# Kernel tuning notes

Measured on AMD Instinct MI355X. Metric: run time of the kernel, lower is better.

## Reference

```python
import jax, jax.numpy as jnp
import numpy as np

B, N, DIM = 4, 2048, 512
H, DH = 8, 64  # heads, dim_head; inner_dim = H*DH = 512


def setup_inputs() -> dict:
    key = jax.random.key(0)
    ks = jax.random.split(key, 7)
    s = 0.02
    return {
        "x": jax.random.normal(ks[0], (B, N, DIM), dtype=jnp.float32),
        "w_qkv": jax.random.normal(ks[1], (DIM, 3 * H * DH), dtype=jnp.float32) * s,
        "b_qkv": jnp.zeros((3 * H * DH,), dtype=jnp.float32),
        "th1": jax.random.normal(ks[2], (H, H), dtype=jnp.float32) * (1.0 / H) + jnp.eye(H, dtype=jnp.float32),
        "th2": jax.random.normal(ks[3], (H, H), dtype=jnp.float32) * (1.0 / H) + jnp.eye(H, dtype=jnp.float32),
        "w_out": jax.random.normal(ks[4], (H * DH, DIM), dtype=jnp.float32) * s,
        "b_out": jnp.zeros((DIM,), dtype=jnp.float32),
    }


def reference(x, w_qkv, b_qkv, th1, th2, w_out, b_out):
    b, n, _ = x.shape
    scale = DH ** -0.5
    qkv = x @ w_qkv + b_qkv                       # [b, n, 3*H*DH]
    q, k, v = jnp.split(qkv, 3, axis=-1)
    to_heads = lambda t: t.reshape(b, n, H, DH).transpose(0, 2, 1, 3)  # b h n d
    q, k, v = to_heads(q), to_heads(k), to_heads(v)
    dots = jnp.einsum('bhnd,bhmd->bhnm', q, k) * scale   # [b, h, n, n]
    dots = jnp.einsum('gh,bhnm->bgnm', th1, dots)        # talking-heads pre-softmax (1x1 conv over heads)
    attn = jax.nn.softmax(dots, axis=-1)
    attn = jnp.einsum('gh,bhnm->bgnm', th2, attn)        # talking-heads post-softmax
    out = jnp.einsum('bhnm,bhmd->bhnd', attn, v)         # [b, h, n, d]
    out = out.transpose(0, 2, 1, 3).reshape(b, n, H * DH)
    return out @ w_out + b_out
```

## Files before the change

### kernel.cpp

```cpp
#include <hip/hip_runtime.h>

typedef _Float16 half8  __attribute__((ext_vector_type(8)));
typedef _Float16 half4  __attribute__((ext_vector_type(4)));
typedef float    f32x4  __attribute__((ext_vector_type(4)));

#define MFMA32(a,b,c) __builtin_amdgcn_mfma_f32_16x16x32_f16(a,b,c,0,0,0)
#define MFMA16(a,b,c) __builtin_amdgcn_mfma_f32_16x16x16f16(a,b,c,0,0,0)

#if __has_builtin(__builtin_amdgcn_exp2f)
#define EXP2F(x) __builtin_amdgcn_exp2f(x)
#else
#define EXP2F(x) exp2f(x)
#endif

#define GLOAD16(gp, lp) __builtin_amdgcn_global_load_lds(                      \
    (const __attribute__((address_space(1))) void*)(gp),                       \
    (__attribute__((address_space(3))) void*)(lp), 16, 0, 0)

static constexpr float SCALE_LOG2E = 0.18033688011112042f;

static constexpr size_t QH_OFF = 0;
static constexpr size_t KH_OFF = (size_t)8  << 20;
static constexpr size_t VT_OFF = (size_t)16 << 20;
static constexpr size_t LS_OFF = (size_t)24 << 20;
static constexpr size_t O_OFF  = (size_t)25 << 20;
static constexpr size_t LPART  = (size_t)4*8*2048;
static constexpr size_t OPART  = (size_t)8192*512;

static constexpr int GS = 340;

__global__ __launch_bounds__(256)
void k_cvtx(const float* __restrict__ x, _Float16* __restrict__ xf)
{
  const size_t i = ((size_t)blockIdx.x*256 + threadIdx.x)*4;
  f32x4 v = *(const f32x4*)(x + i);
  half4 h;
#pragma unroll
  for (int j = 0; j < 4; j++) h[j] = (_Float16)v[j];
  *(half4*)(xf + i) = h;
}

__global__ __launch_bounds__(256)
void k_cvtw(const float* __restrict__ w, _Float16* __restrict__ wt)
{
  __shared__ _Float16 T[32][36];
  const int kt = blockIdx.x, ct = blockIdx.y;
  const int r = threadIdx.x >> 3, c4 = (threadIdx.x & 7)*4;
  f32x4 v = *(const f32x4*)(w + (size_t)(kt*32 + r)*1536 + ct*32 + c4);
#pragma unroll
  for (int j = 0; j < 4; j++) T[r][c4 + j] = (_Float16)v[j];
  __syncthreads();
  half4 o;
#pragma unroll
  for (int j = 0; j < 4; j++) o[j] = T[c4 + j][r];
  *(half4*)(wt + (size_t)(ct*32 + r)*512 + kt*32 + c4) = o;
}

__global__ __launch_bounds__(256)
void k_qkv(const _Float16* __restrict__ xf, const _Float16* __restrict__ wt,
           const float* __restrict__ bias, _Float16* __restrict__ Qh,
           _Float16* __restrict__ Kh, _Float16* __restrict__ Vt)
{
  __shared__ __align__(16) _Float16 Xs[2048];
  __shared__ __align__(16) _Float16 Ws[2048];
  const int tid = threadIdx.x;
  const int wv = tid >> 6, lane = tid & 63, l15 = lane & 15, qd = lane >> 4;
  const int row0 = blockIdx.x * 64, col0 = blockIdx.y * 64;

  const int sslot = wv*64 + lane;
  const int sr = sslot >> 2, so = (sslot & 3) ^ ((sr >> 1) & 3);

  f32x4 acc[4] = {{0.f,0.f,0.f,0.f},{0.f,0.f,0.f,0.f},{0.f,0.f,0.f,0.f},{0.f,0.f,0.f,0.f}};

  for (int k0 = 0; k0 < 512; k0 += 32) {
    GLOAD16(xf + (size_t)(row0 + sr)*512 + k0 + so*8, &Xs[wv*512]);
    GLOAD16(wt + (size_t)(col0 + sr)*512 + k0 + so*8, &Ws[wv*512]);
    __syncthreads();
    const int ra = wv*16 + l15;
    half8 af = *(const half8*)&Xs[(ra*4 + (qd ^ ((ra >> 1) & 3)))*8];
#pragma unroll
    for (int ct = 0; ct < 4; ct++) {
      const int rb = ct*16 + l15;
      half8 bf = *(const half8*)&Ws[(rb*4 + (qd ^ ((rb >> 1) & 3)))*8];
      acc[ct] = MFMA32(af, bf, acc[ct]);
    }
    __syncthreads();
  }
#pragma unroll
  for (int ct = 0; ct < 4; ct++) {
    const int c = col0 + ct*16 + l15;
    const int sec = c >> 9, hh = (c >> 6) & 7, d = c & 63;
    const float bv = bias[c];
#pragma unroll
    for (int i = 0; i < 4; i++) {
      const int row = row0 + wv*16 + qd*4 + i;
      const int bb = row >> 11, n = row & 2047;
      float v = acc[ct][i] + bv;
      if (sec == 0)
        Qh[((size_t)((bb*8 + hh)*2048 + n))*64 + d] = (_Float16)(v * SCALE_LOG2E);
      else if (sec == 1)
        Kh[((size_t)((bb*8 + hh)*2048 + n))*64 + d] = (_Float16)v;
      else
        Vt[((size_t)((bb*8 + hh)*64 + d))*2048 + n] = (_Float16)v;
    }
  }
}

__global__ __launch_bounds__(512, 4)
void k_pass1(const _Float16* __restrict__ Qh, const _Float16* __restrict__ Kh,
             const float* __restrict__ th1, float* __restrict__ Lsum)
{
  __shared__ __align__(16) _Float16 KB[8][1024];
  __shared__ __align__(16) _Float16 Sb[2][2][2704];
  const int tid = threadIdx.x;
  const int wv = tid >> 6, lane = tid & 63, l15 = lane & 15, qd = lane >> 4;
  const int s = blockIdx.x & 7, nt = blockIdx.x >> 3;
  const int b = s >> 1, mh = s & 1;
  const int n0 = nt << 5;
  const _Float16* kbase = Kh + ((size_t)((b*8 + wv)*2048 + mh*1024))*64;

  half4 a1f;
#pragma unroll
  for (int j = 0; j < 4; j++)
    a1f[j] = ((l15 >> 3) == (qd >> 1)) ? (_Float16)th1[(l15 & 7)*8 + (qd & 1)*4 + j]
                                       : (_Float16)0.f;

  half8 qf[2][2];
#pragma unroll
  for (int t = 0; t < 2; t++) {
    const _Float16* qp = Qh + ((size_t)((b*8 + wv)*2048 + n0 + t*16 + l15))*64 + qd*8;
    qf[t][0] = *(const half8*)qp;
    qf[t][1] = *(const half8*)(qp + 32);
  }

  auto issueK = [&](int it) {
#pragma unroll
    for (int j = 0; j < 2; j++) {
      const int bk = j*64 + lane;
      const int m = bk >> 3, c = bk & 7;
      const int cp = c ^ (m & 7);
      GLOAD16(kbase + (size_t)(it*16 + m)*64 + cp*8, &KB[wv][j*512]);
    }
  };
  auto qk_to_sb = [&](int buf) {
    half8 ka0 = *(const half8*)&KB[wv][l15*64 + ((qd       ^ (l15 & 7))*8)];
    half8 ka1 = *(const half8*)&KB[wv][l15*64 + (((4 + qd) ^ (l15 & 7))*8)];
#pragma unroll
    for (int t = 0; t < 2; t++) {
      f32x4 a = {0.f,0.f,0.f,0.f};
      a = MFMA32(ka0, qf[t][0], a);
      a = MFMA32(ka1, qf[t][1], a);
#pragma unroll
      for (int i = 0; i < 4; i++)
        Sb[buf][t][(l15 >> 1)*GS + (qd*4 + i)*20 + wv + 8*(l15 & 1)] = (_Float16)a[i];
    }
  };

  float lacc[2][4];
#pragma unroll
  for (int t = 0; t < 2; t++)
#pragma unroll
    for (int i = 0; i < 4; i++) lacc[t][i] = 0.f;

  issueK(0);
  __syncthreads();
  for (int it = 0; it <= 64; it++) {
    if (it < 64) {
      qk_to_sb(it & 1);
      if (it + 1 < 64) issueK(it + 1);
    }
    if (it >= 1) {
      const int buf = (it - 1) & 1;
#pragma unroll
      for (int t = 0; t < 2; t++) {
        half4 b1 = *(const half4*)&Sb[buf][t][wv*GS + l15*20 + qd*4];
        f32x4 c1 = MFMA16(a1f, b1, ((f32x4){0.f,0.f,0.f,0.f}));
#pragma unroll
        for (int i = 0; i < 4; i++) lacc[t][i] += EXP2F(c1[i]);
      }
    }
    __syncthreads();
  }

#pragma unroll
  for (int t = 0; t < 2; t++)
#pragma unroll
    for (int i = 0; i < 4; i++) {
      float v = lacc[t][i];
      v += __shfl_xor(v, 1); v += __shfl_xor(v, 2);
      v += __shfl_xor(v, 4); v += __shfl_xor(v, 8);
      lacc[t][i] = v;
    }
  if (l15 == 0) {
#pragma unroll
    for (int t = 0; t < 2; t++)
#pragma unroll
      for (int i = 0; i < 4; i++) {
        const int n = n0 + t*16 + wv*2 + (qd >> 1);
        const int g = (qd & 1)*4 + i;
        Lsum[(size_t)mh*LPART + (size_t)(b*8 + g)*2048 + n] = lacc[t][i];
      }
  }
}

__global__ __launch_bounds__(512, 4)
void k_pass2(const _Float16* __restrict__ Qh, const _Float16* __restrict__ Kh,
             const _Float16* __restrict__ Vt, const float* __restrict__ Lsum,
             const float* __restrict__ th1, const float* __restrict__ th2,
             _Float16* __restrict__ Obuf)
{
  __shared__ __align__(16) _Float16 KB[8][1024];
  __shared__ __align__(16) _Float16 VB[8][1024];
  __shared__ __align__(16) _Float16 Sb[2][2][2704];
  __shared__ __align__(16) _Float16 Wb[2][2][2704];
  const int tid = threadIdx.x;
  const int wv = tid >> 6, lane = tid & 63, l15 = lane & 15, qd = lane >> 4;
  const int s = blockIdx.x & 7, nt = blockIdx.x >> 3;
  const int b = s >> 1, mh = s & 1;
  const int n0 = nt << 5;
  const _Float16* kbase = Kh + ((size_t)((b*8 + wv)*2048 + mh*1024))*64;
  const _Float16* vbase = Vt + (size_t)(b*8 + wv)*64*2048 + mh*1024;

  half4 a1f, b2f;
#pragma unroll
  for (int j = 0; j < 4; j++) {
    const bool diag = ((l15 >> 3) == (qd >> 1));
    a1f[j] = diag ? (_Float16)th1[(l15 & 7)*8 + (qd & 1)*4 + j] : (_Float16)0.f;
    b2f[j] = diag ? (_Float16)th2[(l15 & 7)*8 + (qd & 1)*4 + j] : (_Float16)0.f;
  }

  f32x4 cs[2];
#pragma unroll
  for (int t = 0; t < 2; t++)
#pragma unroll
    for (int i = 0; i < 4; i++) {
      const int n = n0 + t*16 + wv*2 + (qd >> 1);
      const int g = (qd & 1)*4 + i;
      const size_t off = (size_t)(b*8 + g)*2048 + n;
      cs[t][i] = -__log2f(Lsum[off] + Lsum[off + LPART]);
    }

  half8 qf[2][2];
#pragma unroll
  for (int t = 0; t < 2; t++) {
    const _Float16* qp = Qh + ((size_t)((b*8 + wv)*2048 + n0 + t*16 + l15))*64 + qd*8;
    qf[t][0] = *(const half8*)qp;
    qf[t][1] = *(const half8*)(qp + 32);
  }

  auto issueK = [&](int it) {
#pragma unroll
    for (int j = 0; j < 2; j++) {
      const int bk = j*64 + lane;
      const int m = bk >> 3, c = bk & 7;
      const int cp = c ^ (m & 7);
      GLOAD16(kbase + (size_t)(it*16 + m)*64 + cp*8, &KB[wv][j*512]);
    }
  };
  auto issueV = [&](int it) {
#pragma unroll
    for (int j = 0; j < 2; j++)
      GLOAD16(vbase + (size_t)lane*2048 + it*16 + j*8, &VB[wv][j*512]);
  };
  auto qk_to_sb = [&](int buf) {
    half8 ka0 = *(const half8*)&KB[wv][l15*64 + ((qd       ^ (l15 & 7))*8)];
    half8 ka1 = *(const half8*)&KB[wv][l15*64 + (((4 + qd) ^ (l15 & 7))*8)];
#pragma unroll
    for (int t = 0; t < 2; t++) {
      f32x4 a = {0.f,0.f,0.f,0.f};
      a = MFMA32(ka0, qf[t][0], a);
      a = MFMA32(ka1, qf[t][1], a);
#pragma unroll
      for (int i = 0; i < 4; i++)
        Sb[buf][t][(l15 >> 1)*GS + (qd*4 + i)*20 + wv + 8*(l15 & 1)] = (_Float16)a[i];
    }
  };

  f32x4 og[2][4];
#pragma unroll
  for (int t = 0; t < 2; t++)
#pragma unroll
    for (int dt = 0; dt < 4; dt++)
      og[t][dt] = (f32x4){0.f,0.f,0.f,0.f};

  issueK(0);
  __syncthreads();

  for (int it = 0; it <= 65; it++) {
    if (it < 64) {
      qk_to_sb(it & 1);
      if (it + 1 < 64) issueK(it + 1);
    }
    if (it >= 1 && it <= 64) {
      const int buf = (it - 1) & 1;
#pragma unroll
      for (int t = 0; t < 2; t++) {
        half4 b1 = *(const half4*)&Sb[buf][t][wv*GS + l15*20 + qd*4];
        f32x4 c1 = MFMA16(a1f, b1, cs[t]);
        half4 a2;
#pragma unroll
        for (int i = 0; i < 4; i++) a2[i] = (_Float16)EXP2F(c1[i]);
        f32x4 c2 = MFMA16(a2, b2f, ((f32x4){0.f,0.f,0.f,0.f}));
        half4 w4;
#pragma unroll
        for (int i = 0; i < 4; i++) w4[i] = (_Float16)c2[i];
        *(half4*)&Wb[buf][t][(l15 & 7)*GS + (wv*2 + (l15 >> 3))*20 + qd*4] = w4;
      }
    }
    if (it >= 2) {
      const int buf = (it - 2) & 1;
      half4 vb[4];
#pragma unroll
      for (int dt = 0; dt < 4; dt++)
        vb[dt] = *(const half4*)&VB[wv][((qd >> 1)*64 + dt*16 + l15)*8 + (qd & 1)*4];
#pragma unroll
      for (int t = 0; t < 2; t++) {
        half4 af = *(const half4*)&Wb[buf][t][wv*GS + l15*20 + qd*4];
#pragma unroll
        for (int dt = 0; dt < 4; dt++)
          og[t][dt] = MFMA16(af, vb[dt], og[t][dt]);
      }
    }
    if (it >= 1 && it <= 64) issueV(it - 1);
    __syncthreads();
  }

  _Float16* Op = Obuf + (size_t)mh * OPART + ((size_t)(b*2048 + n0))*512;
#pragma unroll
  for (int t = 0; t < 2; t++)
#pragma unroll
    for (int dt = 0; dt < 4; dt++)
#pragma unroll
      for (int i = 0; i < 4; i++)
        Op[(size_t)(t*16 + qd*4 + i)*512 + wv*64 + dt*16 + l15] = (_Float16)og[t][dt][i];
}

__global__ __launch_bounds__(256)
void k_oproj(const _Float16* __restrict__ Ob, const float* __restrict__ w,
             const float* __restrict__ bias, float* __restrict__ out)
{
  __shared__ __align__(16) _Float16 Xs[64*40];
  __shared__ __align__(16) _Float16 Wt[64*40];
  const int tid = threadIdx.x;
  const int wv = tid >> 6, lane = tid & 63, l15 = lane & 15, qd = lane >> 4;
  const int row0 = blockIdx.x * 64, col0 = blockIdx.y * 64;
  const int xr = tid >> 2, xc = (tid & 3) * 8;
  const int wk = tid >> 3, wc = (tid & 7) * 8;

  f32x4 acc[4] = {{0.f,0.f,0.f,0.f},{0.f,0.f,0.f,0.f},{0.f,0.f,0.f,0.f},{0.f,0.f,0.f,0.f}};

  for (int k0 = 0; k0 < 512; k0 += 32) {
    const size_t idx = (size_t)(row0 + xr)*512 + k0 + xc;
    half8 a0 = *(const half8*)(Ob + idx);
    half8 a1 = *(const half8*)(Ob + OPART + idx);
    *(half8*)&Xs[xr*40 + xc] = a0 + a1;
    f32x4 b0 = *(const f32x4*)(w + (size_t)(k0 + wk)*512 + col0 + wc);
    f32x4 b1 = *(const f32x4*)(w + (size_t)(k0 + wk)*512 + col0 + wc + 4);
#pragma unroll
    for (int j = 0; j < 4; j++) {
      Wt[(wc+j  )*40 + wk] = (_Float16)b0[j];
      Wt[(wc+j+4)*40 + wk] = (_Float16)b1[j];
    }
    __syncthreads();
    half8 af = *(const half8*)&Xs[(wv*16 + l15)*40 + qd*8];
#pragma unroll
    for (int ct = 0; ct < 4; ct++) {
      half8 bf = *(const half8*)&Wt[(ct*16 + l15)*40 + qd*8];
      acc[ct] = MFMA32(af, bf, acc[ct]);
    }
    __syncthreads();
  }
#pragma unroll
  for (int ct = 0; ct < 4; ct++) {
    const int c = col0 + ct*16 + l15;
    const float bv = bias[c];
#pragma unroll
    for (int i = 0; i < 4; i++) {
      const int row = row0 + wv*16 + qd*4 + i;
      out[(size_t)row*512 + c] = acc[ct][i] + bv;
    }
  }
}

extern "C" void kernel_launch(void* const* d_in, const int* in_sizes, int n_in,
                              void* d_out, int out_size, void* d_ws, size_t ws_size,
                              hipStream_t stream)
{
  (void)in_sizes; (void)n_in; (void)out_size;
  const float* x     = (const float*)d_in[0];
  const float* w_qkv = (const float*)d_in[1];
  const float* b_qkv = (const float*)d_in[2];
  const float* th1   = (const float*)d_in[3];
  const float* th2   = (const float*)d_in[4];
  const float* w_out = (const float*)d_in[5];
  const float* b_out = (const float*)d_in[6];
  float* out = (float*)d_out;

  char* ws = (char*)d_ws;
  _Float16* Qh   = (_Float16*)(ws + QH_OFF);
  _Float16* Kh   = (_Float16*)(ws + KH_OFF);
  _Float16* Vt   = (_Float16*)(ws + VT_OFF);
  float*    Lsum = (float*)   (ws + LS_OFF);
  _Float16* Obuf = (_Float16*)(ws + O_OFF);
  _Float16* Xf   = (_Float16*)(ws + O_OFF);
  _Float16* Wtf  = (_Float16*)(ws + O_OFF + ((size_t)8 << 20));
  if (ws_size < ((size_t)41 << 20)) return;

  k_cvtx <<<dim3(4096),    256, 0, stream>>>(x, Xf);
  k_cvtw <<<dim3(16, 48),  256, 0, stream>>>(w_qkv, Wtf);
  k_qkv  <<<dim3(128, 24), 256, 0, stream>>>(Xf, Wtf, b_qkv, Qh, Kh, Vt);
  k_pass1<<<dim3(512),     512, 0, stream>>>(Qh, Kh, th1, Lsum);
  k_pass2<<<dim3(512),     512, 0, stream>>>(Qh, Kh, Vt, Lsum, th1, th2, Obuf);
  k_oproj<<<dim3(128, 8),  256, 0, stream>>>(Obuf, w_out, b_out, out);
}
```

Baseline: 322.3 us.

## Process two K tiles per barrier in pass1 and issue V loads earlier in pass2

In pass1 the K and score buffers are doubled so each loop iteration handles two 16-key tiles. This halves the number of __syncthreads barriers and lets more global-to-LDS loads be in flight at once. In pass2 the V fragments are read into registers at the top of the iteration and the next V async load is issued earlier, so the load overlaps the QK and softmax work. The cost is roughly double the LDS footprint in pass1, which may lower occupancy under launch_bounds(512,4), and more live registers in pass2.

```diff
diff --git a/kernel.cpp b/kernel.cpp
--- a/kernel.cpp
+++ b/kernel.cpp
@@ -110,8 +110,8 @@
 void k_pass1(const _Float16* __restrict__ Qh, const _Float16* __restrict__ Kh,
              const float* __restrict__ th1, float* __restrict__ Lsum)
 {
-  __shared__ __align__(16) _Float16 KB[8][1024];
-  __shared__ __align__(16) _Float16 Sb[2][2][2704];
+  __shared__ __align__(16) _Float16 KB[2][8][1024];
+  __shared__ __align__(16) _Float16 Sb[2][2][2][2704];
   const int tid = threadIdx.x;
   const int wv = tid >> 6, lane = tid & 63, l15 = lane & 15, qd = lane >> 4;
   const int s = blockIdx.x & 7, nt = blockIdx.x >> 3;
@@ -133,18 +133,18 @@
     qf[t][1] = *(const half8*)(qp + 32);
   }
 
-  auto issueK = [&](int it) {
+  auto issueK = [&](int it, int sub) {
 #pragma unroll
     for (int j = 0; j < 2; j++) {
       const int bk = j*64 + lane;
       const int m = bk >> 3, c = bk & 7;
       const int cp = c ^ (m & 7);
-      GLOAD16(kbase + (size_t)(it*16 + m)*64 + cp*8, &KB[wv][j*512]);
+      GLOAD16(kbase + (size_t)(it*16 + m)*64 + cp*8, &KB[sub][wv][j*512]);
     }
   };
-  auto qk_to_sb = [&](int buf) {
-    half8 ka0 = *(const half8*)&KB[wv][l15*64 + ((qd       ^ (l15 & 7))*8)];
-    half8 ka1 = *(const half8*)&KB[wv][l15*64 + (((4 + qd) ^ (l15 & 7))*8)];
+  auto qk_to_sb = [&](int buf, int sub) {
+    half8 ka0 = *(const half8*)&KB[sub][wv][l15*64 + ((qd       ^ (l15 & 7))*8)];
+    half8 ka1 = *(const half8*)&KB[sub][wv][l15*64 + (((4 + qd) ^ (l15 & 7))*8)];
 #pragma unroll
     for (int t = 0; t < 2; t++) {
       f32x4 a = {0.f,0.f,0.f,0.f};
@@ -152,7 +152,7 @@
       a = MFMA32(ka1, qf[t][1], a);
 #pragma unroll
       for (int i = 0; i < 4; i++)
-        Sb[buf][t][(l15 >> 1)*GS + (qd*4 + i)*20 + wv + 8*(l15 & 1)] = (_Float16)a[i];
+        Sb[buf][sub][t][(l15 >> 1)*GS + (qd*4 + i)*20 + wv + 8*(l15 & 1)] = (_Float16)a[i];
     }
   };
 
@@ -162,22 +162,29 @@
 #pragma unroll
     for (int i = 0; i < 4; i++) lacc[t][i] = 0.f;
 
-  issueK(0);
+  issueK(0, 0);
+  issueK(1, 1);
   __syncthreads();
-  for (int it = 0; it <= 64; it++) {
-    if (it < 64) {
-      qk_to_sb(it & 1);
-      if (it + 1 < 64) issueK(it + 1);
-    }
-    if (it >= 1) {
-      const int buf = (it - 1) & 1;
-#pragma unroll
-      for (int t = 0; t < 2; t++) {
-        half4 b1 = *(const half4*)&Sb[buf][t][wv*GS + l15*20 + qd*4];
-        f32x4 c1 = MFMA16(a1f, b1, ((f32x4){0.f,0.f,0.f,0.f}));
-#pragma unroll
-        for (int i = 0; i < 4; i++) lacc[t][i] += EXP2F(c1[i]);
+  for (int ot = 0; ot <= 32; ot++) {
+    if (ot < 32) {
+      qk_to_sb(ot & 1, 0);
+      qk_to_sb(ot & 1, 1);
+      if (ot + 1 < 32) {
+        issueK(2*ot + 2, 0);
+        issueK(2*ot + 3, 1);
       }
+    }
+    if (ot >= 1) {
+      const int buf = (ot - 1) & 1;
+#pragma unroll
+      for (int sub = 0; sub < 2; sub++)
+#pragma unroll
+        for (int t = 0; t < 2; t++) {
+          half4 b1 = *(const half4*)&Sb[buf][sub][t][wv*GS + l15*20 + qd*4];
+          f32x4 c1 = MFMA16(a1f, b1, ((f32x4){0.f,0.f,0.f,0.f}));
+#pragma unroll
+          for (int i = 0; i < 4; i++) lacc[t][i] += EXP2F(c1[i]);
+        }
     }
     __syncthreads();
   }
@@ -287,10 +294,19 @@
   __syncthreads();
 
   for (int it = 0; it <= 65; it++) {
+    half4 vb[4];
+    if (it >= 2) {
+#pragma unroll
+      for (int dt = 0; dt < 4; dt++)
+        vb[dt] = *(const half4*)&VB[wv][((qd >> 1)*64 + dt*16 + l15)*8 + (qd & 1)*4];
+    }
+    if (it >= 1 && it <= 64) issueV(it - 1);
+
     if (it < 64) {
       qk_to_sb(it & 1);
       if (it + 1 < 64) issueK(it + 1);
     }
+
     if (it >= 1 && it <= 64) {
       const int buf = (it - 1) & 1;
 #pragma unroll
@@ -309,10 +325,6 @@
     }
     if (it >= 2) {
       const int buf = (it - 2) & 1;
-      half4 vb[4];
-#pragma unroll
-      for (int dt = 0; dt < 4; dt++)
-        vb[dt] = *(const half4*)&VB[wv][((qd >> 1)*64 + dt*16 + l15)*8 + (qd & 1)*4];
 #pragma unroll
       for (int t = 0; t < 2; t++) {
         half4 af = *(const half4*)&Wb[buf][t][wv*GS + l15*20 + qd*4];
@@ -321,7 +333,6 @@
           og[t][dt] = MFMA16(af, vb[dt], og[t][dt]);
       }
     }
-    if (it >= 1 && it <= 64) issueV(it - 1);
     __syncthreads();
   }
 
```

Measured after the change: 324.2 us. About the same (+0.6%).
